# Kernel tuning notes

Hardware: AMD Instinct MI355X
Metric: run time of the kernel (lower is better)

Reference implementation:

```python
import jax, jax.numpy as jnp
import numpy as np

B, N, M = 2, 8192, 8192
PEN_RATIO = 0.95
REG_W = 0.001
LOSS_W = 1.0
EPS_COS = 1e-8


def quat_to_rot(q):
    # q: [..., 4] in (x, y, z, w) order (legacy kornia convention), assumed normalized
    x, y, z, w = q[..., 0], q[..., 1], q[..., 2], q[..., 3]
    r0 = jnp.stack([1 - 2 * (y * y + z * z), 2 * (x * y - z * w), 2 * (x * z + y * w)], -1)
    r1 = jnp.stack([2 * (x * y + z * w), 1 - 2 * (x * x + z * z), 2 * (y * z - x * w)], -1)
    r2 = jnp.stack([2 * (x * z - y * w), 2 * (y * z + x * w), 1 - 2 * (x * x + y * y)], -1)
    return jnp.stack([r0, r1, r2], -2)


def span_cov(cp):
    # cp: [N,7] -> SPD cov [N,3,3]; eigenvalues are cumulative sums (e0, e0+e1, e0+e1+e2)
    e0 = cp[:, 0]
    e1 = e0 + cp[:, 1]
    e2 = e1 + cp[:, 2]
    eig = jnp.stack([e0, e1, e2], -1)  # [N,3]
    q = cp[:, 3:] / (jnp.linalg.norm(cp[:, 3:], axis=-1, keepdims=True) + 1e-9)
    E = quat_to_rot(q)  # [N,3,3]
    return jnp.einsum('nij,nj,nkj->nik', E, eig, E)


def setup_inputs() -> dict:
    key = jax.random.key(0)
    ks = jax.random.split(key, 8)
    return {
        'xyz_pred': jax.random.normal(ks[0], (B, N, 3), jnp.float32) * 10.0,
        'xyz_target': jax.random.normal(ks[1], (B, M, 3), jnp.float32) * 10.0,
        'cov_pred': jax.random.uniform(ks[2], (B, N, 7), jnp.float32),
        'cov_target': jax.random.uniform(ks[3], (B, M, 7), jnp.float32),
        'R_pred': jax.random.normal(ks[4], (B, 3, 3), jnp.float32),
        't_pred': jax.random.normal(ks[5], (B, 3), jnp.float32),
        'normal_pred': jax.random.normal(ks[6], (B, N, 3), jnp.float32),
        'normal_target': jax.random.normal(ks[7], (B, M, 3), jnp.float32),
    }


def reference(xyz_pred, xyz_target, cov_pred, cov_target, R_pred, t_pred, normal_pred, normal_target):
    def per_batch(xp, xt, cp, ct, R, nrm):
        covp = span_cov(cp)  # [N,3,3]
        covt = span_cov(ct)  # [M,3,3]
        # one-direction chamfer: squared NN distance + index (||p||^2+||t||^2-2 p.t)
        d2 = (xp * xp).sum(-1)[:, None] + (xt * xt).sum(-1)[None, :] - 2.0 * (xp @ xt.T)  # [N,M]
        diff = d2.min(axis=1)          # [N]
        idx = jnp.argmin(d2, axis=1)   # [N]
        xa = xt[idx]                   # associated target points
        cpa = covt[idx]                # associated target covariances
        dv = xp - xa
        # ROI mask via kth value: k = 1 + int(N*ratio) (1-indexed) -> sorted[int(N*ratio)]
        m = jnp.maximum(jnp.sort(diff)[int(N * PEN_RATIO)], 1.0)
        cm = (diff < m).astype(xp.dtype)
        nvalid = cm.sum()
        Rd = jax.lax.stop_gradient(R)
        sigma = covp + jnp.einsum('ij,njk,lk->nil', Rd, cpa, Rd)
        sigma_inv = jnp.linalg.inv(sigma)
        sq = jnp.einsum('ni,nij,nj->n', dv, sigma_inv, dv)  # Mahalanobis sq dist
        logdet = jnp.log(jnp.linalg.det(sigma))
        loss_b = (sq * cm).sum() / nvalid + REG_W * (0.5 * logdet * cm).sum() / nvalid
        # weighted SVD registration head (single ICP iter), all detached as in torch
        diff_na = xa - xp
        cossim = (nrm * diff_na).sum(-1) / jnp.maximum(
            jnp.linalg.norm(nrm, axis=-1) * jnp.linalg.norm(diff_na, axis=-1), EPS_COS)
        w = jax.lax.stop_gradient(jnp.abs(cossim) ** 2 * cm)
        src = jax.lax.stop_gradient(xp)
        tgt = jax.lax.stop_gradient(xa)
        wn = w / w.sum()
        sc = (wn[:, None] * src).sum(0)
        tc = (wn[:, None] * tgt).sum(0)
        H = jnp.einsum('n,ni,nj->ij', w, src - sc, tgt - tc)
        U, S, Vt = jnp.linalg.svd(H)
        V = Vt.T
        d = jnp.linalg.det(V @ U.T)
        Rres = V @ jnp.diag(jnp.stack([jnp.ones_like(d), jnp.ones_like(d), d])) @ U.T
        tres = tc - Rres @ sc
        return loss_b, Rres, tres

    losses, Rs, ts = jax.vmap(per_batch)(xyz_pred, xyz_target, cov_pred, cov_target, R_pred, normal_pred)
    return LOSS_W * losses.sum(), Rs, ts
```

## Files before the change

kernel.cpp:

```cpp
#include <hip/hip_runtime.h>
#include <math.h>

#define B_ 2
#define N_ 8192
#define M_ 8192
#define KSEL 7782
#define CH 128
#define CHS (M_ / CH)
#define PTS 1024

__device__ __forceinline__ unsigned ord_of(float f) {
  unsigned u = __float_as_uint(f);
  return (u & 0x80000000u) ? ~u : (u | 0x80000000u);
}
__device__ __forceinline__ float float_of_ord(unsigned o) {
  unsigned u = (o & 0x80000000u) ? (o ^ 0x80000000u) : ~o;
  return __uint_as_float(u);
}

__global__ __launch_bounds__(256) void init_kernel(
    unsigned long long* __restrict__ keys, const float* __restrict__ xt,
    float* __restrict__ tnorm) {
  const int gid = blockIdx.x * 256 + threadIdx.x;
  keys[gid] = 0xFFFFFFFFFFFFFFFFull;
  float tx = xt[gid * 3 + 0], ty = xt[gid * 3 + 1], tz = xt[gid * 3 + 2];
  tnorm[gid] = tx * tx + ty * ty + tz * tz;
}

__global__ __launch_bounds__(256, 8) void nn_kernel(
    const float* __restrict__ xp, const float* __restrict__ xt,
    const float* __restrict__ tnorm, unsigned long long* __restrict__ keys) {
  const int b = blockIdx.z;
  const int pblk = blockIdx.x;
  const int ch = blockIdx.y;

  __shared__ float4 tg[CHS];
  const float* __restrict__ xtb = xt + ((size_t)b * M_ + (size_t)ch * CHS) * 3;
  const float* __restrict__ twb = tnorm + (size_t)b * M_ + (size_t)ch * CHS;
  if (threadIdx.x < CHS) {
    const int j = threadIdx.x;
    tg[j] = make_float4(xtb[3 * j + 0], xtb[3 * j + 1], xtb[3 * j + 2],
                        twb[j]);
  }
  __syncthreads();

  const int i0 = pblk * PTS + threadIdx.x;
  float xm[4], ym[4], zm[4], nrm2[4], best[4];
  int bi[4];
#pragma unroll
  for (int k = 0; k < 4; ++k) {
    const float* p = xp + ((size_t)b * N_ + i0 + k * 256) * 3;
    float x = p[0], y = p[1], z = p[2];
    nrm2[k] = x * x + y * y + z * z;
    xm[k] = -2.0f * x;
    ym[k] = -2.0f * y;
    zm[k] = -2.0f * z;
    best[k] = 3.4e38f;
    bi[k] = 0;
  }

#pragma unroll 2
  for (int j = 0; j < CHS; ++j) {
    float4 t = tg[j];
#pragma unroll
    for (int k = 0; k < 4; ++k) {
      float d = fmaf(t.x, xm[k], fmaf(t.y, ym[k], fmaf(t.z, zm[k], t.w)));
      if (d < best[k]) { best[k] = d; bi[k] = j; }
    }
  }

  const int base = ch * CHS;
#pragma unroll
  for (int k = 0; k < 4; ++k) {
    unsigned long long key =
        ((unsigned long long)ord_of(best[k] + nrm2[k]) << 32) |
        (unsigned)(base + bi[k]);
    atomicMin(&keys[(size_t)b * N_ + i0 + k * 256], key);
  }
}

__global__ __launch_bounds__(1024) void sel_kernel(
    const unsigned long long* __restrict__ keys, float* __restrict__ mout,
    double* __restrict__ acc) {
  __shared__ unsigned hist[256];
  __shared__ unsigned sel_digit, sel_rank;
  const int b = blockIdx.x;

  if (threadIdx.x < 32) acc[b * 32 + threadIdx.x] = 0.0;

  unsigned v[8];
#pragma unroll
  for (int t = 0; t < 8; ++t)
    v[t] = (unsigned)(keys[(size_t)b * N_ + threadIdx.x + t * 1024] >> 32);

  unsigned prefix = 0;
  unsigned rank = KSEL;

#pragma unroll
  for (int pass = 0; pass < 4; ++pass) {
    const int shift = 24 - pass * 8;
    const unsigned pmask = (pass == 0) ? 0u : (0xFFFFFFFFu << (shift + 8));

    if (threadIdx.x < 256) hist[threadIdx.x] = 0;
    __syncthreads();

#pragma unroll
    for (int t = 0; t < 8; ++t) {
      if ((v[t] & pmask) == prefix)
        atomicAdd(&hist[(v[t] >> shift) & 0xFFu], 1u);
    }
    __syncthreads();

    if (threadIdx.x < 64) {
      const int lane = threadIdx.x;
      unsigned h0 = hist[lane * 4 + 0], h1 = hist[lane * 4 + 1];
      unsigned h2 = hist[lane * 4 + 2], h3 = hist[lane * 4 + 3];
      unsigned c0 = h0, c1 = c0 + h1, c2 = c1 + h2, c3 = c2 + h3;
      unsigned s = c3;
#pragma unroll
      for (int off = 1; off < 64; off <<= 1) {
        unsigned t = __shfl_up(s, off);
        if (lane >= off) s += t;
      }
      unsigned excl = s - c3;
      unsigned r = rank;
      if (r >= excl && r < excl + c0) { sel_digit = lane * 4 + 0; sel_rank = r - excl; }
      if (r >= excl + c0 && r < excl + c1) { sel_digit = lane * 4 + 1; sel_rank = r - (excl + c0); }
      if (r >= excl + c1 && r < excl + c2) { sel_digit = lane * 4 + 2; sel_rank = r - (excl + c1); }
      if (r >= excl + c2 && r < excl + c3) { sel_digit = lane * 4 + 3; sel_rank = r - (excl + c2); }
    }
    __syncthreads();
    prefix |= (sel_digit << shift);
    rank = sel_rank;
    __syncthreads();
  }

  if (threadIdx.x == 0) {
    float f = float_of_ord(prefix);
    mout[b] = fmaxf(f, 1.0f);
  }
}

__device__ __forceinline__ void cov_from_params(const float* __restrict__ c,
                                                float C[3][3]) {
  float e0 = c[0];
  float e1 = e0 + c[1];
  float e2 = e1 + c[2];
  float qx = c[3], qy = c[4], qz = c[5], qw = c[6];
  float qn = sqrtf(qx * qx + qy * qy + qz * qz + qw * qw) + 1e-9f;
  float x = qx / qn, y = qy / qn, z = qz / qn, w = qw / qn;
  float E[3][3];
  E[0][0] = 1.0f - 2.0f * (y * y + z * z);
  E[0][1] = 2.0f * (x * y - z * w);
  E[0][2] = 2.0f * (x * z + y * w);
  E[1][0] = 2.0f * (x * y + z * w);
  E[1][1] = 1.0f - 2.0f * (x * x + z * z);
  E[1][2] = 2.0f * (y * z - x * w);
  E[2][0] = 2.0f * (x * z - y * w);
  E[2][1] = 2.0f * (y * z + x * w);
  E[2][2] = 1.0f - 2.0f * (x * x + y * y);
#pragma unroll
  for (int i = 0; i < 3; ++i)
#pragma unroll
    for (int k = 0; k < 3; ++k)
      C[i][k] = e0 * E[i][0] * E[k][0] + e1 * E[i][1] * E[k][1] +
                e2 * E[i][2] * E[k][2];
}

__global__ __launch_bounds__(256) void main_kernel(
    const float* __restrict__ xp, const float* __restrict__ xt,
    const float* __restrict__ cpp, const float* __restrict__ ctp,
    const float* __restrict__ Rp, const float* __restrict__ nrm,
    const unsigned long long* __restrict__ keys, const float* __restrict__ mout,
    double* __restrict__ acc) {
  const int b = blockIdx.y;
  const int i = blockIdx.x * 256 + threadIdx.x;

  float R[3][3];
#pragma unroll
  for (int r = 0; r < 3; ++r)
#pragma unroll
    for (int c = 0; c < 3; ++c) R[r][c] = Rp[b * 9 + r * 3 + c];
  const float m = mout[b];

  unsigned long long key = keys[(size_t)b * N_ + i];
  float d2 = float_of_ord((unsigned)(key >> 32));
  int id = (int)(key & 0xFFFFFFFFull);

  const float* p = xp + ((size_t)b * N_ + i) * 3;
  float px = p[0], py = p[1], pz = p[2];
  const float* a_ = xt + ((size_t)b * M_ + id) * 3;
  float ax = a_[0], ay = a_[1], az = a_[2];

  float cmv = (d2 < m) ? 1.0f : 0.0f;

  float Cp[3][3], Ct[3][3];
  cov_from_params(cpp + ((size_t)b * N_ + i) * 7, Cp);
  cov_from_params(ctp + ((size_t)b * M_ + id) * 7, Ct);

  float T[3][3], G[3][3];
#pragma unroll
  for (int r = 0; r < 3; ++r)
#pragma unroll
    for (int c = 0; c < 3; ++c)
      T[r][c] = R[r][0] * Ct[0][c] + R[r][1] * Ct[1][c] + R[r][2] * Ct[2][c];
#pragma unroll
  for (int r = 0; r < 3; ++r)
#pragma unroll
    for (int c = 0; c < 3; ++c)
      G[r][c] = Cp[r][c] +
                (T[r][0] * R[c][0] + T[r][1] * R[c][1] + T[r][2] * R[c][2]);

  float c00 = G[1][1] * G[2][2] - G[1][2] * G[2][1];
  float c01 = G[1][2] * G[2][0] - G[1][0] * G[2][2];
  float c02 = G[1][0] * G[2][1] - G[1][1] * G[2][0];
  float det = G[0][0] * c00 + G[0][1] * c01 + G[0][2] * c02;
  float rdet = 1.0f / det;
  float i00 = (G[1][1] * G[2][2] - G[1][2] * G[2][1]) * rdet;
  float i01 = (G[0][2] * G[2][1] - G[0][1] * G[2][2]) * rdet;
  float i02 = (G[0][1] * G[1][2] - G[0][2] * G[1][1]) * rdet;
  float i10 = (G[1][2] * G[2][0] - G[1][0] * G[2][2]) * rdet;
  float i11 = (G[0][0] * G[2][2] - G[0][2] * G[2][0]) * rdet;
  float i12 = (G[0][2] * G[1][0] - G[0][0] * G[1][2]) * rdet;
  float i20 = (G[1][0] * G[2][1] - G[1][1] * G[2][0]) * rdet;
  float i21 = (G[0][1] * G[2][0] - G[0][0] * G[2][1]) * rdet;
  float i22 = (G[0][0] * G[1][1] - G[0][1] * G[1][0]) * rdet;

  float dvx = px - ax, dvy = py - ay, dvz = pz - az;
  float t0 = i00 * dvx + i01 * dvy + i02 * dvz;
  float t1 = i10 * dvx + i11 * dvy + i12 * dvz;
  float t2 = i20 * dvx + i21 * dvy + i22 * dvz;
  float sq = dvx * t0 + dvy * t1 + dvz * t2;
  float logdet = logf(det);

  const float* nv = nrm + ((size_t)b * N_ + i) * 3;
  float nx = nv[0], ny = nv[1], nz = nv[2];
  float gx = ax - px, gy = ay - py, gz = az - pz;
  float dt = nx * gx + ny * gy + nz * gz;
  float den = fmaxf(sqrtf(nx * nx + ny * ny + nz * nz) *
                        sqrtf(gx * gx + gy * gy + gz * gz),
                    1e-8f);
  float cs = dt / den;
  float w = cs * cs * cmv;

  double vals[19];
  vals[0] = (double)cmv;
  vals[1] = (double)(sq) * (double)cmv;
  vals[2] = (double)(logdet) * (double)cmv;
  vals[3] = (double)w;
  vals[4] = (double)w * px;
  vals[5] = (double)w * py;
  vals[6] = (double)w * pz;
  vals[7] = (double)w * ax;
  vals[8] = (double)w * ay;
  vals[9] = (double)w * az;
  float pr[3] = {px, py, pz}, ar[3] = {ax, ay, az};
#pragma unroll
  for (int r = 0; r < 3; ++r)
#pragma unroll
    for (int c = 0; c < 3; ++c)
      vals[10 + r * 3 + c] = (double)w * (double)pr[r] * (double)ar[c];

#pragma unroll
  for (int off = 32; off > 0; off >>= 1) {
#pragma unroll
    for (int k = 0; k < 19; ++k) vals[k] += __shfl_down(vals[k], off);
  }
  __shared__ double red[4][19];
  const int lane = threadIdx.x & 63, wv = threadIdx.x >> 6;
  if (lane == 0) {
#pragma unroll
    for (int k = 0; k < 19; ++k) red[wv][k] = vals[k];
  }
  __syncthreads();
  if (threadIdx.x < 19) {
    double s = red[0][threadIdx.x] + red[1][threadIdx.x] +
               red[2][threadIdx.x] + red[3][threadIdx.x];
    atomicAdd(&acc[b * 32 + threadIdx.x], s);
  }
}

__device__ double det3(const double M[3][3]) {
  return M[0][0] * (M[1][1] * M[2][2] - M[1][2] * M[2][1]) -
         M[0][1] * (M[1][0] * M[2][2] - M[1][2] * M[2][0]) +
         M[0][2] * (M[1][0] * M[2][1] - M[1][1] * M[2][0]);
}

__device__ void eigvec3(const double A[3][3], double lam, double v[3]) {
  double r[3][3];
#pragma unroll
  for (int i = 0; i < 3; ++i) {
#pragma unroll
    for (int j = 0; j < 3; ++j) r[i][j] = A[i][j];
    r[i][i] -= lam;
  }
  double c01[3] = {r[0][1] * r[1][2] - r[0][2] * r[1][1],
                   r[0][2] * r[1][0] - r[0][0] * r[1][2],
                   r[0][0] * r[1][1] - r[0][1] * r[1][0]};
  double c02[3] = {r[0][1] * r[2][2] - r[0][2] * r[2][1],
                   r[0][2] * r[2][0] - r[0][0] * r[2][2],
                   r[0][0] * r[2][1] - r[0][1] * r[2][0]};
  double c12[3] = {r[1][1] * r[2][2] - r[1][2] * r[2][1],
                   r[1][2] * r[2][0] - r[1][0] * r[2][2],
                   r[1][0] * r[2][1] - r[1][1] * r[2][0]};
  double n01 = c01[0] * c01[0] + c01[1] * c01[1] + c01[2] * c01[2];
  double n02 = c02[0] * c02[0] + c02[1] * c02[1] + c02[2] * c02[2];
  double n12 = c12[0] * c12[0] + c12[1] * c12[1] + c12[2] * c12[2];
  double* best = c01;
  double bn = n01;
  if (n02 > bn) { best = c02; bn = n02; }
  if (n12 > bn) { best = c12; bn = n12; }
  double inv = (bn > 0.0) ? 1.0 / sqrt(bn) : 0.0;
  v[0] = best[0] * inv;
  v[1] = best[1] * inv;
  v[2] = best[2] * inv;
  if (inv == 0.0) v[0] = 1.0;
}

__device__ void kabsch(const double H[3][3], double R[3][3]) {
  double A[3][3];
  for (int i = 0; i < 3; ++i)
    for (int j = 0; j < 3; ++j)
      A[i][j] = H[0][i] * H[0][j] + H[1][i] * H[1][j] + H[2][i] * H[2][j];

  double lam[3];
  double Vs[3][3];
  double mtr = (A[0][0] + A[1][1] + A[2][2]) / 3.0;
  double K00 = A[0][0] - mtr, K11 = A[1][1] - mtr, K22 = A[2][2] - mtr;
  double a01 = A[0][1], a02 = A[0][2], a12 = A[1][2];
  double p2 = K00 * K00 + K11 * K11 + K22 * K22 +
              2.0 * (a01 * a01 + a02 * a02 + a12 * a12);
  double p = sqrt(p2 / 6.0);
  if (p < 1e-100) {
    lam[0] = lam[1] = lam[2] = mtr;
    for (int i = 0; i < 3; ++i)
      for (int j = 0; j < 3; ++j) Vs[i][j] = (i == j) ? 1.0 : 0.0;
  } else {
    double detK = K00 * (K11 * K22 - a12 * a12) -
                  a01 * (a01 * K22 - a12 * a02) +
                  a02 * (a01 * a12 - K11 * a02);
    double rr = detK / (2.0 * p * p * p);
    rr = fmin(1.0, fmax(-1.0, rr));
    double phi = acos(rr) / 3.0;
    lam[0] = mtr + 2.0 * p * cos(phi);
    lam[2] = mtr + 2.0 * p * cos(phi + 2.0943951023931953);
    lam[1] = 3.0 * mtr - lam[0] - lam[2];

    double v0[3], v1[3];
    eigvec3(A, lam[0], v0);
    eigvec3(A, lam[1], v1);
    double dp = v1[0] * v0[0] + v1[1] * v0[1] + v1[2] * v0[2];
    v1[0] -= dp * v0[0];
    v1[1] -= dp * v0[1];
    v1[2] -= dp * v0[2];
    double n1 = v1[0] * v1[0] + v1[1] * v1[1] + v1[2] * v1[2];
    if (n1 > 1e-200) {
      double inv = 1.0 / sqrt(n1);
      v1[0] *= inv; v1[1] *= inv; v1[2] *= inv;
    } else {
      double ax = fabs(v0[0]), ay = fabs(v0[1]), az = fabs(v0[2]);
      double t[3] = {0, 0, 0};
      if (ax <= ay && ax <= az) t[0] = 1.0;
      else if (ay <= az) t[1] = 1.0;
      else t[2] = 1.0;
      v1[0] = v0[1] * t[2] - v0[2] * t[1];
      v1[1] = v0[2] * t[0] - v0[0] * t[2];
      v1[2] = v0[0] * t[1] - v0[1] * t[0];
      double inv = 1.0 / sqrt(v1[0] * v1[0] + v1[1] * v1[1] + v1[2] * v1[2]);
      v1[0] *= inv; v1[1] *= inv; v1[2] *= inv;
    }
    double v2[3] = {v0[1] * v1[2] - v0[2] * v1[1],
                    v0[2] * v1[0] - v0[0] * v1[2],
                    v0[0] * v1[1] - v0[1] * v1[0]};
    for (int i = 0; i < 3; ++i) {
      Vs[i][0] = v0[i];
      Vs[i][1] = v1[i];
      Vs[i][2] = v2[i];
    }
  }

  double sg[3];
  for (int c = 0; c < 3; ++c) sg[c] = sqrt(fmax(lam[c], 0.0));

  double U[3][3];
  for (int c = 0; c < 3; ++c) {
    double ux = H[0][0] * Vs[0][c] + H[0][1] * Vs[1][c] + H[0][2] * Vs[2][c];
    double uy = H[1][0] * Vs[0][c] + H[1][1] * Vs[1][c] + H[1][2] * Vs[2][c];
    double uz = H[2][0] * Vs[0][c] + H[2][1] * Vs[1][c] + H[2][2] * Vs[2][c];
    double inv = (sg[c] > 1e-12 * sg[0] + 1e-300) ? 1.0 / sg[c] : 0.0;
    U[0][c] = ux * inv;
    U[1][c] = uy * inv;
    U[2][c] = uz * inv;
  }
  if (sg[2] <= 1e-12 * sg[0] + 1e-300) {
    U[0][2] = U[1][0] * U[2][1] - U[2][0] * U[1][1];
    U[1][2] = U[2][0] * U[0][1] - U[0][0] * U[2][1];
    U[2][2] = U[0][0] * U[1][1] - U[1][0] * U[0][1];
  }
  double d = det3(U) * det3(Vs);
  for (int i = 0; i < 3; ++i)
    for (int j = 0; j < 3; ++j)
      R[i][j] = Vs[i][0] * U[j][0] + Vs[i][1] * U[j][1] + d * Vs[i][2] * U[j][2];
}

__global__ __launch_bounds__(64) void finalize_kernel(
    const double* __restrict__ acc, float* __restrict__ out) {
  __shared__ double lossb[B_];
  const int b = threadIdx.x;
  if (b < B_) {
    const double* a = acc + b * 32;
    double cnt = a[0], ssq = a[1], sld = a[2], W = a[3];
    double loss = ssq / cnt + 0.001 * 0.5 * sld / cnt;
    lossb[b] = loss;
    double Ss[3] = {a[4], a[5], a[6]}, St[3] = {a[7], a[8], a[9]};
    double sc[3], tc[3];
    for (int c = 0; c < 3; ++c) { sc[c] = Ss[c] / W; tc[c] = St[c] / W; }
    double H[3][3];
    for (int i = 0; i < 3; ++i)
      for (int j = 0; j < 3; ++j)
        H[i][j] = a[10 + i * 3 + j] - Ss[i] * St[j] / W;
    double Rm[3][3];
    kabsch(H, Rm);
    for (int i = 0; i < 3; ++i)
      for (int j = 0; j < 3; ++j)
        out[1 + b * 9 + i * 3 + j] = (float)Rm[i][j];
    for (int i = 0; i < 3; ++i) {
      double t =
          tc[i] - (Rm[i][0] * sc[0] + Rm[i][1] * sc[1] + Rm[i][2] * sc[2]);
      out[1 + B_ * 9 + b * 3 + i] = (float)t;
    }
  }
  __syncthreads();
  if (threadIdx.x == 0) out[0] = (float)(lossb[0] + lossb[1]);
}

extern "C" void kernel_launch(void* const* d_in, const int* in_sizes, int n_in,
                              void* d_out, int out_size, void* d_ws,
                              size_t ws_size, hipStream_t stream) {
  const float* xyz_pred = (const float*)d_in[0];
  const float* xyz_target = (const float*)d_in[1];
  const float* cov_pred = (const float*)d_in[2];
  const float* cov_target = (const float*)d_in[3];
  const float* R_pred = (const float*)d_in[4];
  const float* normal_pred = (const float*)d_in[6];
  float* out = (float*)d_out;

  char* ws = (char*)d_ws;
  double* acc = (double*)ws;
  unsigned long long* keys = (unsigned long long*)(ws + 512);
  float* mout = (float*)(ws + 512 + (size_t)B_ * N_ * 8);
  float* tnorm = (float*)(ws + 1024 + (size_t)B_ * N_ * 8);

  hipLaunchKernelGGL(init_kernel, dim3(B_ * M_ / 256), dim3(256), 0, stream,
                     keys, xyz_target, tnorm);
  hipLaunchKernelGGL(nn_kernel, dim3(N_ / PTS, CH, B_), dim3(256), 0, stream,
                     xyz_pred, xyz_target, tnorm, keys);
  hipLaunchKernelGGL(sel_kernel, dim3(B_), dim3(1024), 0, stream, keys, mout,
                     acc);
  hipLaunchKernelGGL(main_kernel, dim3(N_ / 256, B_), dim3(256), 0, stream,
                     xyz_pred, xyz_target, cov_pred, cov_target, R_pred,
                     normal_pred, keys, mout, acc);
  hipLaunchKernelGGL(finalize_kernel, dim3(1), dim3(64), 0, stream, acc, out);
}
```

Measured before the change: 45.72 us.

## Replace atomicMin NN reduction with per-segment partial keys and merge kernel

Instead of initializing a key buffer and having every target-chunk block atomicMin its result, each block now writes its per-segment minimum key into a partial buffer, and a new merge kernel reduces over 64 segments. Target norms are computed inline in the NN kernel, which removes the init kernel, and the accumulator reset moves into the merge kernel. Segment count drops from 128 to 64 with a larger loop unroll. This trades the contention of 64-bit atomics for an extra 8 MB of partial traffic and one more strided-read pass.

New measurement: 50.99 us. +11.5%, slower.

```diff
diff --git a/kernel.cpp b/kernel.cpp
--- a/kernel.cpp
+++ b/kernel.cpp
@@ -5,8 +5,8 @@
 #define N_ 8192
 #define M_ 8192
 #define KSEL 7782
-#define CH 128
-#define CHS (M_ / CH)
+#define S_ 64
+#define SEG (M_ / S_)
 #define PTS 1024
 
 __device__ __forceinline__ unsigned ord_of(float f) {
@@ -18,29 +18,19 @@
   return __uint_as_float(u);
 }
 
-__global__ __launch_bounds__(256) void init_kernel(
-    unsigned long long* __restrict__ keys, const float* __restrict__ xt,
-    float* __restrict__ tnorm) {
-  const int gid = blockIdx.x * 256 + threadIdx.x;
-  keys[gid] = 0xFFFFFFFFFFFFFFFFull;
-  float tx = xt[gid * 3 + 0], ty = xt[gid * 3 + 1], tz = xt[gid * 3 + 2];
-  tnorm[gid] = tx * tx + ty * ty + tz * tz;
-}
-
 __global__ __launch_bounds__(256, 8) void nn_kernel(
     const float* __restrict__ xp, const float* __restrict__ xt,
-    const float* __restrict__ tnorm, unsigned long long* __restrict__ keys) {
+    unsigned long long* __restrict__ part) {
   const int b = blockIdx.z;
   const int pblk = blockIdx.x;
-  const int ch = blockIdx.y;
-
-  __shared__ float4 tg[CHS];
-  const float* __restrict__ xtb = xt + ((size_t)b * M_ + (size_t)ch * CHS) * 3;
-  const float* __restrict__ twb = tnorm + (size_t)b * M_ + (size_t)ch * CHS;
-  if (threadIdx.x < CHS) {
+  const int s = blockIdx.y;
+
+  __shared__ float4 tg[SEG];
+  const float* __restrict__ xtb = xt + ((size_t)b * M_ + (size_t)s * SEG) * 3;
+  if (threadIdx.x < SEG) {
     const int j = threadIdx.x;
-    tg[j] = make_float4(xtb[3 * j + 0], xtb[3 * j + 1], xtb[3 * j + 2],
-                        twb[j]);
+    float tx = xtb[3 * j + 0], ty = xtb[3 * j + 1], tz = xtb[3 * j + 2];
+    tg[j] = make_float4(tx, ty, tz, tx * tx + ty * ty + tz * tz);
   }
   __syncthreads();
 
@@ -59,8 +49,8 @@
     bi[k] = 0;
   }
 
-#pragma unroll 2
-  for (int j = 0; j < CHS; ++j) {
+#pragma unroll 4
+  for (int j = 0; j < SEG; ++j) {
     float4 t = tg[j];
 #pragma unroll
     for (int k = 0; k < 4; ++k) {
@@ -69,24 +59,37 @@
     }
   }
 
-  const int base = ch * CHS;
+  const int base = s * SEG;
+  unsigned long long* dst = part + ((size_t)(b * S_ + s)) * N_ + i0;
 #pragma unroll
   for (int k = 0; k < 4; ++k) {
-    unsigned long long key =
-        ((unsigned long long)ord_of(best[k] + nrm2[k]) << 32) |
-        (unsigned)(base + bi[k]);
-    atomicMin(&keys[(size_t)b * N_ + i0 + k * 256], key);
-  }
+    dst[k * 256] = ((unsigned long long)ord_of(best[k] + nrm2[k]) << 32) |
+                   (unsigned)(base + bi[k]);
+  }
+}
+
+__global__ __launch_bounds__(256) void merge_kernel(
+    const unsigned long long* __restrict__ part,
+    unsigned long long* __restrict__ keys, double* __restrict__ acc) {
+  const int gid = blockIdx.x * 256 + threadIdx.x;
+  const int b = gid >> 13;
+  const int n = gid & (N_ - 1);
+  const unsigned long long* src = part + (size_t)b * S_ * N_ + n;
+  unsigned long long best = src[0];
+#pragma unroll 8
+  for (int s = 1; s < S_; ++s) {
+    unsigned long long v = src[(size_t)s * N_];
+    if (v < best) best = v;
+  }
+  keys[gid] = best;
+  if (gid < B_ * 32) acc[gid] = 0.0;
 }
 
 __global__ __launch_bounds__(1024) void sel_kernel(
-    const unsigned long long* __restrict__ keys, float* __restrict__ mout,
-    double* __restrict__ acc) {
+    const unsigned long long* __restrict__ keys, float* __restrict__ mout) {
   __shared__ unsigned hist[256];
   __shared__ unsigned sel_digit, sel_rank;
   const int b = blockIdx.x;
-
-  if (threadIdx.x < 32) acc[b * 32 + threadIdx.x] = 0.0;
 
   unsigned v[8];
 #pragma unroll
@@ -446,17 +449,18 @@
   float* out = (float*)d_out;
 
   char* ws = (char*)d_ws;
-  double* acc = (double*)ws;
-  unsigned long long* keys = (unsigned long long*)(ws + 512);
-  float* mout = (float*)(ws + 512 + (size_t)B_ * N_ * 8);
-  float* tnorm = (float*)(ws + 1024 + (size_t)B_ * N_ * 8);
-
-  hipLaunchKernelGGL(init_kernel, dim3(B_ * M_ / 256), dim3(256), 0, stream,
-                     keys, xyz_target, tnorm);
-  hipLaunchKernelGGL(nn_kernel, dim3(N_ / PTS, CH, B_), dim3(256), 0, stream,
-                     xyz_pred, xyz_target, tnorm, keys);
-  hipLaunchKernelGGL(sel_kernel, dim3(B_), dim3(1024), 0, stream, keys, mout,
-                     acc);
+  unsigned long long* part = (unsigned long long*)ws;
+  size_t part_bytes = (size_t)B_ * S_ * N_ * 8;
+  double* acc = (double*)(ws + part_bytes);
+  unsigned long long* keys =
+      (unsigned long long*)(ws + part_bytes + 512);
+  float* mout = (float*)(ws + part_bytes + 512 + (size_t)B_ * N_ * 8);
+
+  hipLaunchKernelGGL(nn_kernel, dim3(N_ / PTS, S_, B_), dim3(256), 0, stream,
+                     xyz_pred, xyz_target, part);
+  hipLaunchKernelGGL(merge_kernel, dim3(B_ * N_ / 256), dim3(256), 0, stream,
+                     part, keys, acc);
+  hipLaunchKernelGGL(sel_kernel, dim3(B_), dim3(1024), 0, stream, keys, mout);
   hipLaunchKernelGGL(main_kernel, dim3(N_ / 256, B_), dim3(256), 0, stream,
                      xyz_pred, xyz_target, cov_pred, cov_target, R_pred,
                      normal_pred, keys, mout, acc);
```

## Fuse finalize into main kernel, inline target norms, and raise NN points per thread

Applied to the files above, without the earlier changes.

Folds the finalize kernel into main_kernel using a last-block-done atomic counter, which removes one launch. The target squared norms are now computed inside nn_kernel's shared-memory load instead of in init_kernel, and accumulator zeroing moves into init_kernel. Each NN thread now handles 8 query points instead of 4, with PTS doubled and unroll raised, to improve reuse of each shared-memory target load. The cost is higher register pressure, which lowers the occupancy bound to 4, and halves the number of NN blocks.

After: 51.75 us. 1.13x slower.

```diff
diff --git a/kernel.cpp b/kernel.cpp
--- a/kernel.cpp
+++ b/kernel.cpp
@@ -7,7 +7,8 @@
 #define KSEL 7782
 #define CH 128
 #define CHS (M_ / CH)
-#define PTS 1024
+#define PTS 2048
+#define PPT 8
 
 __device__ __forceinline__ unsigned ord_of(float f) {
   unsigned u = __float_as_uint(f);
@@ -19,36 +20,35 @@
 }
 
 __global__ __launch_bounds__(256) void init_kernel(
-    unsigned long long* __restrict__ keys, const float* __restrict__ xt,
-    float* __restrict__ tnorm) {
+    unsigned long long* __restrict__ keys, double* __restrict__ acc,
+    unsigned* __restrict__ done) {
   const int gid = blockIdx.x * 256 + threadIdx.x;
   keys[gid] = 0xFFFFFFFFFFFFFFFFull;
-  float tx = xt[gid * 3 + 0], ty = xt[gid * 3 + 1], tz = xt[gid * 3 + 2];
-  tnorm[gid] = tx * tx + ty * ty + tz * tz;
-}
-
-__global__ __launch_bounds__(256, 8) void nn_kernel(
+  if (gid < B_ * 32) acc[gid] = 0.0;
+  if (gid == 0) *done = 0u;
+}
+
+__global__ __launch_bounds__(256, 4) void nn_kernel(
     const float* __restrict__ xp, const float* __restrict__ xt,
-    const float* __restrict__ tnorm, unsigned long long* __restrict__ keys) {
+    unsigned long long* __restrict__ keys) {
   const int b = blockIdx.z;
   const int pblk = blockIdx.x;
   const int ch = blockIdx.y;
 
   __shared__ float4 tg[CHS];
   const float* __restrict__ xtb = xt + ((size_t)b * M_ + (size_t)ch * CHS) * 3;
-  const float* __restrict__ twb = tnorm + (size_t)b * M_ + (size_t)ch * CHS;
   if (threadIdx.x < CHS) {
     const int j = threadIdx.x;
-    tg[j] = make_float4(xtb[3 * j + 0], xtb[3 * j + 1], xtb[3 * j + 2],
-                        twb[j]);
+    float tx = xtb[3 * j + 0], ty = xtb[3 * j + 1], tz = xtb[3 * j + 2];
+    tg[j] = make_float4(tx, ty, tz, tx * tx + ty * ty + tz * tz);
   }
   __syncthreads();
 
   const int i0 = pblk * PTS + threadIdx.x;
-  float xm[4], ym[4], zm[4], nrm2[4], best[4];
-  int bi[4];
-#pragma unroll
-  for (int k = 0; k < 4; ++k) {
+  float xm[PPT], ym[PPT], zm[PPT], nrm2[PPT], best[PPT];
+  int bi[PPT];
+#pragma unroll
+  for (int k = 0; k < PPT; ++k) {
     const float* p = xp + ((size_t)b * N_ + i0 + k * 256) * 3;
     float x = p[0], y = p[1], z = p[2];
     nrm2[k] = x * x + y * y + z * z;
@@ -59,11 +59,11 @@
     bi[k] = 0;
   }
 
-#pragma unroll 2
+#pragma unroll 4
   for (int j = 0; j < CHS; ++j) {
     float4 t = tg[j];
 #pragma unroll
-    for (int k = 0; k < 4; ++k) {
+    for (int k = 0; k < PPT; ++k) {
       float d = fmaf(t.x, xm[k], fmaf(t.y, ym[k], fmaf(t.z, zm[k], t.w)));
       if (d < best[k]) { best[k] = d; bi[k] = j; }
     }
@@ -71,7 +71,7 @@
 
   const int base = ch * CHS;
 #pragma unroll
-  for (int k = 0; k < 4; ++k) {
+  for (int k = 0; k < PPT; ++k) {
     unsigned long long key =
         ((unsigned long long)ord_of(best[k] + nrm2[k]) << 32) |
         (unsigned)(base + bi[k]);
@@ -80,13 +80,10 @@
 }
 
 __global__ __launch_bounds__(1024) void sel_kernel(
-    const unsigned long long* __restrict__ keys, float* __restrict__ mout,
-    double* __restrict__ acc) {
+    const unsigned long long* __restrict__ keys, float* __restrict__ mout) {
   __shared__ unsigned hist[256];
   __shared__ unsigned sel_digit, sel_rank;
   const int b = blockIdx.x;
-
-  if (threadIdx.x < 32) acc[b * 32 + threadIdx.x] = 0.0;
 
   unsigned v[8];
 #pragma unroll
@@ -165,119 +162,6 @@
     for (int k = 0; k < 3; ++k)
       C[i][k] = e0 * E[i][0] * E[k][0] + e1 * E[i][1] * E[k][1] +
                 e2 * E[i][2] * E[k][2];
-}
-
-__global__ __launch_bounds__(256) void main_kernel(
-    const float* __restrict__ xp, const float* __restrict__ xt,
-    const float* __restrict__ cpp, const float* __restrict__ ctp,
-    const float* __restrict__ Rp, const float* __restrict__ nrm,
-    const unsigned long long* __restrict__ keys, const float* __restrict__ mout,
-    double* __restrict__ acc) {
-  const int b = blockIdx.y;
-  const int i = blockIdx.x * 256 + threadIdx.x;
-
-  float R[3][3];
-#pragma unroll
-  for (int r = 0; r < 3; ++r)
-#pragma unroll
-    for (int c = 0; c < 3; ++c) R[r][c] = Rp[b * 9 + r * 3 + c];
-  const float m = mout[b];
-
-  unsigned long long key = keys[(size_t)b * N_ + i];
-  float d2 = float_of_ord((unsigned)(key >> 32));
-  int id = (int)(key & 0xFFFFFFFFull);
-
-  const float* p = xp + ((size_t)b * N_ + i) * 3;
-  float px = p[0], py = p[1], pz = p[2];
-  const float* a_ = xt + ((size_t)b * M_ + id) * 3;
-  float ax = a_[0], ay = a_[1], az = a_[2];
-
-  float cmv = (d2 < m) ? 1.0f : 0.0f;
-
-  float Cp[3][3], Ct[3][3];
-  cov_from_params(cpp + ((size_t)b * N_ + i) * 7, Cp);
-  cov_from_params(ctp + ((size_t)b * M_ + id) * 7, Ct);
-
-  float T[3][3], G[3][3];
-#pragma unroll
-  for (int r = 0; r < 3; ++r)
-#pragma unroll
-    for (int c = 0; c < 3; ++c)
-      T[r][c] = R[r][0] * Ct[0][c] + R[r][1] * Ct[1][c] + R[r][2] * Ct[2][c];
-#pragma unroll
-  for (int r = 0; r < 3; ++r)
-#pragma unroll
-    for (int c = 0; c < 3; ++c)
-      G[r][c] = Cp[r][c] +
-                (T[r][0] * R[c][0] + T[r][1] * R[c][1] + T[r][2] * R[c][2]);
-
-  float c00 = G[1][1] * G[2][2] - G[1][2] * G[2][1];
-  float c01 = G[1][2] * G[2][0] - G[1][0] * G[2][2];
-  float c02 = G[1][0] * G[2][1] - G[1][1] * G[2][0];
-  float det = G[0][0] * c00 + G[0][1] * c01 + G[0][2] * c02;
-  float rdet = 1.0f / det;
-  float i00 = (G[1][1] * G[2][2] - G[1][2] * G[2][1]) * rdet;
-  float i01 = (G[0][2] * G[2][1] - G[0][1] * G[2][2]) * rdet;
-  float i02 = (G[0][1] * G[1][2] - G[0][2] * G[1][1]) * rdet;
-  float i10 = (G[1][2] * G[2][0] - G[1][0] * G[2][2]) * rdet;
-  float i11 = (G[0][0] * G[2][2] - G[0][2] * G[2][0]) * rdet;
-  float i12 = (G[0][2] * G[1][0] - G[0][0] * G[1][2]) * rdet;
-  float i20 = (G[1][0] * G[2][1] - G[1][1] * G[2][0]) * rdet;
-  float i21 = (G[0][1] * G[2][0] - G[0][0] * G[2][1]) * rdet;
-  float i22 = (G[0][0] * G[1][1] - G[0][1] * G[1][0]) * rdet;
-
-  float dvx = px - ax, dvy = py - ay, dvz = pz - az;
-  float t0 = i00 * dvx + i01 * dvy + i02 * dvz;
-  float t1 = i10 * dvx + i11 * dvy + i12 * dvz;
-  float t2 = i20 * dvx + i21 * dvy + i22 * dvz;
-  float sq = dvx * t0 + dvy * t1 + dvz * t2;
-  float logdet = logf(det);
-
-  const float* nv = nrm + ((size_t)b * N_ + i) * 3;
-  float nx = nv[0], ny = nv[1], nz = nv[2];
-  float gx = ax - px, gy = ay - py, gz = az - pz;
-  float dt = nx * gx + ny * gy + nz * gz;
-  float den = fmaxf(sqrtf(nx * nx + ny * ny + nz * nz) *
-                        sqrtf(gx * gx + gy * gy + gz * gz),
-                    1e-8f);
-  float cs = dt / den;
-  float w = cs * cs * cmv;
-
-  double vals[19];
-  vals[0] = (double)cmv;
-  vals[1] = (double)(sq) * (double)cmv;
-  vals[2] = (double)(logdet) * (double)cmv;
-  vals[3] = (double)w;
-  vals[4] = (double)w * px;
-  vals[5] = (double)w * py;
-  vals[6] = (double)w * pz;
-  vals[7] = (double)w * ax;
-  vals[8] = (double)w * ay;
-  vals[9] = (double)w * az;
-  float pr[3] = {px, py, pz}, ar[3] = {ax, ay, az};
-#pragma unroll
-  for (int r = 0; r < 3; ++r)
-#pragma unroll
-    for (int c = 0; c < 3; ++c)
-      vals[10 + r * 3 + c] = (double)w * (double)pr[r] * (double)ar[c];
-
-#pragma unroll
-  for (int off = 32; off > 0; off >>= 1) {
-#pragma unroll
-    for (int k = 0; k < 19; ++k) vals[k] += __shfl_down(vals[k], off);
-  }
-  __shared__ double red[4][19];
-  const int lane = threadIdx.x & 63, wv = threadIdx.x >> 6;
-  if (lane == 0) {
-#pragma unroll
-    for (int k = 0; k < 19; ++k) red[wv][k] = vals[k];
-  }
-  __syncthreads();
-  if (threadIdx.x < 19) {
-    double s = red[0][threadIdx.x] + red[1][threadIdx.x] +
-               red[2][threadIdx.x] + red[3][threadIdx.x];
-    atomicAdd(&acc[b * 32 + threadIdx.x], s);
-  }
 }
 
 __device__ double det3(const double M[3][3]) {
@@ -403,31 +287,154 @@
       R[i][j] = Vs[i][0] * U[j][0] + Vs[i][1] * U[j][1] + d * Vs[i][2] * U[j][2];
 }
 
-__global__ __launch_bounds__(64) void finalize_kernel(
-    const double* __restrict__ acc, float* __restrict__ out) {
+__global__ __launch_bounds__(256) void main_kernel(
+    const float* __restrict__ xp, const float* __restrict__ xt,
+    const float* __restrict__ cpp, const float* __restrict__ ctp,
+    const float* __restrict__ Rp, const float* __restrict__ nrm,
+    const unsigned long long* __restrict__ keys, const float* __restrict__ mout,
+    double* __restrict__ acc, unsigned* __restrict__ done,
+    float* __restrict__ out) {
+  const int b = blockIdx.y;
+  const int i = blockIdx.x * 256 + threadIdx.x;
+
+  float R[3][3];
+#pragma unroll
+  for (int r = 0; r < 3; ++r)
+#pragma unroll
+    for (int c = 0; c < 3; ++c) R[r][c] = Rp[b * 9 + r * 3 + c];
+  const float m = mout[b];
+
+  unsigned long long key = keys[(size_t)b * N_ + i];
+  float d2 = float_of_ord((unsigned)(key >> 32));
+  int id = (int)(key & 0xFFFFFFFFull);
+
+  const float* p = xp + ((size_t)b * N_ + i) * 3;
+  float px = p[0], py = p[1], pz = p[2];
+  const float* a_ = xt + ((size_t)b * M_ + id) * 3;
+  float ax = a_[0], ay = a_[1], az = a_[2];
+
+  float cmv = (d2 < m) ? 1.0f : 0.0f;
+
+  float Cp[3][3], Ct[3][3];
+  cov_from_params(cpp + ((size_t)b * N_ + i) * 7, Cp);
+  cov_from_params(ctp + ((size_t)b * M_ + id) * 7, Ct);
+
+  float T[3][3], G[3][3];
+#pragma unroll
+  for (int r = 0; r < 3; ++r)
+#pragma unroll
+    for (int c = 0; c < 3; ++c)
+      T[r][c] = R[r][0] * Ct[0][c] + R[r][1] * Ct[1][c] + R[r][2] * Ct[2][c];
+#pragma unroll
+  for (int r = 0; r < 3; ++r)
+#pragma unroll
+    for (int c = 0; c < 3; ++c)
+      G[r][c] = Cp[r][c] +
+                (T[r][0] * R[c][0] + T[r][1] * R[c][1] + T[r][2] * R[c][2]);
+
+  float c00 = G[1][1] * G[2][2] - G[1][2] * G[2][1];
+  float c01 = G[1][2] * G[2][0] - G[1][0] * G[2][2];
+  float c02 = G[1][0] * G[2][1] - G[1][1] * G[2][0];
+  float det = G[0][0] * c00 + G[0][1] * c01 + G[0][2] * c02;
+  float rdet = 1.0f / det;
+  float i00 = (G[1][1] * G[2][2] - G[1][2] * G[2][1]) * rdet;
+  float i01 = (G[0][2] * G[2][1] - G[0][1] * G[2][2]) * rdet;
+  float i02 = (G[0][1] * G[1][2] - G[0][2] * G[1][1]) * rdet;
+  float i10 = (G[1][2] * G[2][0] - G[1][0] * G[2][2]) * rdet;
+  float i11 = (G[0][0] * G[2][2] - G[0][2] * G[2][0]) * rdet;
+  float i12 = (G[0][2] * G[1][0] - G[0][0] * G[1][2]) * rdet;
+  float i20 = (G[1][0] * G[2][1] - G[1][1] * G[2][0]) * rdet;
+  float i21 = (G[0][1] * G[2][0] - G[0][0] * G[2][1]) * rdet;
+  float i22 = (G[0][0] * G[1][1] - G[0][1] * G[1][0]) * rdet;
+
+  float dvx = px - ax, dvy = py - ay, dvz = pz - az;
+  float t0 = i00 * dvx + i01 * dvy + i02 * dvz;
+  float t1 = i10 * dvx + i11 * dvy + i12 * dvz;
+  float t2 = i20 * dvx + i21 * dvy + i22 * dvz;
+  float sq = dvx * t0 + dvy * t1 + dvz * t2;
+  float logdet = logf(det);
+
+  const float* nv = nrm + ((size_t)b * N_ + i) * 3;
+  float nx = nv[0], ny = nv[1], nz = nv[2];
+  float gx = ax - px, gy = ay - py, gz = az - pz;
+  float dt = nx * gx + ny * gy + nz * gz;
+  float den = fmaxf(sqrtf(nx * nx + ny * ny + nz * nz) *
+                        sqrtf(gx * gx + gy * gy + gz * gz),
+                    1e-8f);
+  float cs = dt / den;
+  float w = cs * cs * cmv;
+
+  double vals[19];
+  vals[0] = (double)cmv;
+  vals[1] = (double)(sq) * (double)cmv;
+  vals[2] = (double)(logdet) * (double)cmv;
+  vals[3] = (double)w;
+  vals[4] = (double)w * px;
+  vals[5] = (double)w * py;
+  vals[6] = (double)w * pz;
+  vals[7] = (double)w * ax;
+  vals[8] = (double)w * ay;
+  vals[9] = (double)w * az;
+  float pr[3] = {px, py, pz}, ar[3] = {ax, ay, az};
+#pragma unroll
+  for (int r = 0; r < 3; ++r)
+#pragma unroll
+    for (int c = 0; c < 3; ++c)
+      vals[10 + r * 3 + c] = (double)w * (double)pr[r] * (double)ar[c];
+
+#pragma unroll
+  for (int off = 32; off > 0; off >>= 1) {
+#pragma unroll
+    for (int k = 0; k < 19; ++k) vals[k] += __shfl_down(vals[k], off);
+  }
+  __shared__ double red[4][19];
+  const int lane = threadIdx.x & 63, wv = threadIdx.x >> 6;
+  if (lane == 0) {
+#pragma unroll
+    for (int k = 0; k < 19; ++k) red[wv][k] = vals[k];
+  }
+  __syncthreads();
+  if (threadIdx.x < 19) {
+    double s = red[0][threadIdx.x] + red[1][threadIdx.x] +
+               red[2][threadIdx.x] + red[3][threadIdx.x];
+    atomicAdd(&acc[b * 32 + threadIdx.x], s);
+  }
+
+  __shared__ bool amLast;
+  __threadfence();
+  if (threadIdx.x == 0) {
+    unsigned old = atomicAdd(done, 1u);
+    amLast = (old == gridDim.x * gridDim.y - 1);
+  }
+  __syncthreads();
+  if (!amLast) return;
+  __threadfence();
+
   __shared__ double lossb[B_];
-  const int b = threadIdx.x;
-  if (b < B_) {
-    const double* a = acc + b * 32;
+  const int fb = threadIdx.x;
+  if (fb < B_) {
+    double a[19];
+#pragma unroll
+    for (int k = 0; k < 19; ++k)
+      a[k] = atomicAdd(&acc[fb * 32 + k], 0.0);
     double cnt = a[0], ssq = a[1], sld = a[2], W = a[3];
-    double loss = ssq / cnt + 0.001 * 0.5 * sld / cnt;
-    lossb[b] = loss;
+    lossb[fb] = ssq / cnt + 0.001 * 0.5 * sld / cnt;
     double Ss[3] = {a[4], a[5], a[6]}, St[3] = {a[7], a[8], a[9]};
     double sc[3], tc[3];
     for (int c = 0; c < 3; ++c) { sc[c] = Ss[c] / W; tc[c] = St[c] / W; }
     double H[3][3];
-    for (int i = 0; i < 3; ++i)
-      for (int j = 0; j < 3; ++j)
-        H[i][j] = a[10 + i * 3 + j] - Ss[i] * St[j] / W;
+    for (int r = 0; r < 3; ++r)
+      for (int c = 0; c < 3; ++c)
+        H[r][c] = a[10 + r * 3 + c] - Ss[r] * St[c] / W;
     double Rm[3][3];
     kabsch(H, Rm);
-    for (int i = 0; i < 3; ++i)
-      for (int j = 0; j < 3; ++j)
-        out[1 + b * 9 + i * 3 + j] = (float)Rm[i][j];
-    for (int i = 0; i < 3; ++i) {
+    for (int r = 0; r < 3; ++r)
+      for (int c = 0; c < 3; ++c)
+        out[1 + fb * 9 + r * 3 + c] = (float)Rm[r][c];
+    for (int r = 0; r < 3; ++r) {
       double t =
-          tc[i] - (Rm[i][0] * sc[0] + Rm[i][1] * sc[1] + Rm[i][2] * sc[2]);
-      out[1 + B_ * 9 + b * 3 + i] = (float)t;
+          tc[r] - (Rm[r][0] * sc[0] + Rm[r][1] * sc[1] + Rm[r][2] * sc[2]);
+      out[1 + B_ * 9 + fb * 3 + r] = (float)t;
     }
   }
   __syncthreads();
@@ -447,18 +454,16 @@
 
   char* ws = (char*)d_ws;
   double* acc = (double*)ws;
-  unsigned long long* keys = (unsigned long long*)(ws + 512);
-  float* mout = (float*)(ws + 512 + (size_t)B_ * N_ * 8);
-  float* tnorm = (float*)(ws + 1024 + (size_t)B_ * N_ * 8);
-
-  hipLaunchKernelGGL(init_kernel, dim3(B_ * M_ / 256), dim3(256), 0, stream,
-                     keys, xyz_target, tnorm);
+  unsigned* done = (unsigned*)(ws + 512);
+  unsigned long long* keys = (unsigned long long*)(ws + 1024);
+  float* mout = (float*)(ws + 1024 + (size_t)B_ * N_ * 8);
+
+  hipLaunchKernelGGL(init_kernel, dim3(B_ * N_ / 256), dim3(256), 0, stream,
+                     keys, acc, done);
   hipLaunchKernelGGL(nn_kernel, dim3(N_ / PTS, CH, B_), dim3(256), 0, stream,
-                     xyz_pred, xyz_target, tnorm, keys);
-  hipLaunchKernelGGL(sel_kernel, dim3(B_), dim3(1024), 0, stream, keys, mout,
-                     acc);
+                     xyz_pred, xyz_target, keys);
+  hipLaunchKernelGGL(sel_kernel, dim3(B_), dim3(1024), 0, stream, keys, mout);
   hipLaunchKernelGGL(main_kernel, dim3(N_ / 256, B_), dim3(256), 0, stream,
                      xyz_pred, xyz_target, cov_pred, cov_target, R_pred,
-                     normal_pred, keys, mout, acc);
-  hipLaunchKernelGGL(finalize_kernel, dim3(1), dim3(64), 0, stream, acc, out);
-}
+                     normal_pred, keys, mout, acc, done, out);
+}
```
